# Optimization experiments

Hardware: AMD Instinct MI355X
Metric: run time of the kernel (lower is better)

## Reference

```python
import jax, jax.numpy as jnp
import numpy as np

G_GRID, K_SPLINE = 8, 3          # KAN grid size and spline order (k=3 in source)
N_GRAPHS = 512                    # graphs in the batched graph
NEG_SLOPE = 0.01                  # nn.LeakyReLU default

def _knots():
    # pykan-style grid on [-1,1] extended by k knots each side
    h = 2.0 / G_GRID
    base = jnp.linspace(-1.0, 1.0, G_GRID + 1)
    lo = -1.0 - h * jnp.arange(K_SPLINE, 0, -1, dtype=jnp.float32)
    hi = 1.0 + h * jnp.arange(1, K_SPLINE + 1, dtype=jnp.float32)
    return jnp.concatenate([lo, base, hi])  # [G + 2k + 1]

def _bspline(x, knots):
    # Cox-de Boor recursion. x: [N, D] -> basis [N, D, G + k]
    xx = x[..., None]
    b = ((xx >= knots[:-1]) & (xx < knots[1:])).astype(x.dtype)
    for d in range(1, K_SPLINE + 1):
        left = (xx - knots[:-(d + 1)]) / (knots[d:-1] - knots[:-(d + 1)]) * b[..., :-1]
        right = (knots[d + 1:] - xx) / (knots[d + 1:] - knots[1:-d]) * b[..., 1:]
        b = left + right
    return b

def _kan_layer(x, coef, sb, ss, knots):
    # phi(x)_o = sum_i sb[i,o]*silu(x_i) + ss[i,o]*sum_c coef[i,o,c]*B_c(x_i)
    B = _bspline(x, knots)                               # [N, in, C]
    return jnp.einsum('nic,ioc->no', B, coef * ss[:, :, None]) + jax.nn.silu(x) @ sb

def setup_inputs() -> dict:
    key = jax.random.key(0)
    ks = jax.random.split(key, 24)
    N, E, IN, HID, OUT, MID, C = 100000, 1600000, 64, 128, 1, 5, G_GRID + K_SPLINE
    def p(k, shape, s=0.1):
        return jax.random.normal(k, shape, jnp.float32) * s
    inp = {}
    inp['h'] = jax.random.normal(ks[0], (N, IN), jnp.float32) * 0.5
    inp['src'] = jax.random.randint(ks[1], (E,), 0, N)
    inp['dst'] = jax.random.randint(ks[2], (E,), 0, N)
    inp['gid'] = jnp.sort(jax.random.randint(ks[3], (N,), 0, N_GRAPHS))
    # KAN encoder: width=[IN, 5, HID]
    inp['coef1'] = p(ks[4], (IN, MID, C)); inp['sb1'] = p(ks[5], (IN, MID)); inp['ss1'] = p(ks[6], (IN, MID))
    inp['coef2'] = p(ks[7], (MID, HID, C)); inp['sb2'] = p(ks[8], (MID, HID)); inp['ss2'] = p(ks[9], (MID, HID))
    # two SAGEConv('mean') layers
    inp['Ws0'] = p(ks[10], (HID, HID)); inp['Wn0'] = p(ks[11], (HID, HID)); inp['b0'] = jnp.zeros((HID,), jnp.float32)
    inp['Ws1'] = p(ks[12], (HID, HID)); inp['Wn1'] = p(ks[13], (HID, HID)); inp['b1'] = jnp.zeros((HID,), jnp.float32)
    # KAN readout: width=[HID, 5, OUT]
    inp['coefr1'] = p(ks[14], (HID, MID, C)); inp['sbr1'] = p(ks[15], (HID, MID)); inp['ssr1'] = p(ks[16], (HID, MID))
    inp['coefr2'] = p(ks[17], (MID, OUT, C)); inp['sbr2'] = p(ks[18], (MID, OUT)); inp['ssr2'] = p(ks[19], (MID, OUT))
    return inp

def reference(h, src, dst, gid, coef1, sb1, ss1, coef2, sb2, ss2,
              Ws0, Wn0, b0, Ws1, Wn1, b1,
              coefr1, sbr1, ssr1, coefr2, sbr2, ssr2):
    knots = _knots()
    N = h.shape[0]
    # KAN spline encoder: [N, IN] -> [N, 5] -> [N, HID]
    h = _kan_layer(_kan_layer(h, coef1, sb1, ss1, knots), coef2, sb2, ss2, knots)
    # in-degree for mean aggregation (zero-degree nodes get 0 neighbor message)
    deg = jnp.maximum(jax.ops.segment_sum(jnp.ones(src.shape, h.dtype), dst, num_segments=N), 1.0)[:, None]
    for Ws, Wn, b in ((Ws0, Wn0, b0), (Ws1, Wn1, b1)):
        mean_n = jax.ops.segment_sum(h[src], dst, num_segments=N) / deg   # gather + mean-scatter
        z = h @ Ws + mean_n @ Wn + b + h                                   # SAGEConv + residual
        h = jnp.where(z > 0, z, NEG_SLOPE * z)                             # leaky_relu
    # average pooling per graph
    cnt = jnp.maximum(jax.ops.segment_sum(jnp.ones((N,), h.dtype), gid, num_segments=N_GRAPHS), 1.0)[:, None]
    y = jax.ops.segment_sum(h, gid, num_segments=N_GRAPHS) / cnt           # [G, HID]
    # KAN readout + sigmoid
    y = _kan_layer(_kan_layer(y, coefr1, sbr1, ssr1, knots), coefr2, sbr2, ssr2, knots)
    return jax.nn.sigmoid(y)
```

## Files before the change

### kernel.cpp

```cpp
#include <hip/hip_runtime.h>


#define IN_F   64
#define MID_F  5
#define HID_F  128
#define NG     512
#define NC     11
#define NJ     14
#define NXCD   8
#define PGRID  1024

typedef __attribute__((ext_vector_type(8))) __bf16 bf16x8;
typedef __attribute__((ext_vector_type(4))) float  f32x4;

__device__ __forceinline__ void bspline11(float x, float* __restrict__ B) {
    float b[14];
#pragma unroll
    for (int j = 0; j < 14; ++j) {
        float tj = -1.75f + 0.25f * j;
        b[j] = (x >= tj && x < tj + 0.25f) ? 1.0f : 0.0f;
    }
#pragma unroll
    for (int d = 1; d <= 3; ++d) {
        float inv = 1.0f / (0.25f * d);
#pragma unroll 14
        for (int j = 0; j < 14 - 3; ++j) {
            if (j < 14 - d) {
                float tj   = -1.75f + 0.25f * j;
                float tjd1 = tj + 0.25f * (d + 1);
                b[j] = ((x - tj) * b[j] + (tjd1 - x) * b[j + 1]) * inv;
            }
        }
        if (d < 3) {
#pragma unroll
            for (int j = 11; j < 14; ++j) {
                if (j < 14 - d) {
                    float tj   = -1.75f + 0.25f * j;
                    float tjd1 = tj + 0.25f * (d + 1);
                    b[j] = ((x - tj) * b[j] + (tjd1 - x) * b[j + 1]) * inv;
                }
            }
        }
    }
#pragma unroll
    for (int j = 0; j < NC; ++j) B[j] = b[j];
}

__device__ __forceinline__ float silu_f(float x) { return x / (1.0f + expf(-x)); }

__device__ __forceinline__ float4 poly_from_coefs(float c0, float c1, float c2, float c3) {
    const float s = 1.0f / 6.0f;
    float4 p;
    p.x = (-c0 + 3.f*c1 - 3.f*c2 + c3) * s;
    p.y = ( 3.f*c0 - 6.f*c1 + 3.f*c2) * s;
    p.z = (-3.f*c0 + 3.f*c2) * s;
    p.w = (      c0 + 4.f*c1 + c2) * s;
    return p;
}

__global__ __launch_bounds__(256) void build_poly1_kernel(
    const float* __restrict__ coef1, const float* __restrict__ ss1,
    float* __restrict__ poly1)
{
    int idx = blockIdx.x * 256 + threadIdx.x;
    if (idx >= IN_F * NJ * MID_F) return;
    int o = idx % MID_F;
    int t = idx / MID_F;
    int j = t % NJ;
    int i = t / NJ;
    float ss = ss1[i * MID_F + o];
    float c[4];
#pragma unroll
    for (int k = 0; k < 4; ++k) {
        int cc = j - 3 + k;
        c[k] = (cc >= 0 && cc <= 10) ? coef1[(i * MID_F + o) * NC + cc] * ss : 0.f;
    }
    *(float4*)(poly1 + (size_t)idx * 4) = poly_from_coefs(c[0], c[1], c[2], c[3]);
}

__global__ __launch_bounds__(256) void build_poly2_kernel(
    const float* __restrict__ coef2, const float* __restrict__ ss2,
    float* __restrict__ poly2)
{
    int idx = blockIdx.x * 256 + threadIdx.x;
    if (idx >= MID_F * NJ * HID_F) return;
    int o = idx & 127;
    int t = idx >> 7;
    int j = t % NJ;
    int i = t / NJ;
    float ss = ss2[i * HID_F + o];
    float c[4];
#pragma unroll
    for (int k = 0; k < 4; ++k) {
        int cc = j - 3 + k;
        c[k] = (cc >= 0 && cc <= 10) ? coef2[(i * HID_F + o) * NC + cc] * ss : 0.f;
    }
    *(float4*)(poly2 + (size_t)idx * 4) = poly_from_coefs(c[0], c[1], c[2], c[3]);
}

__global__ __launch_bounds__(256) void build_wfrag_kernel(
    const float* __restrict__ Ws0, const float* __restrict__ Wn0,
    const float* __restrict__ Ws1, const float* __restrict__ Wn1,
    unsigned short* __restrict__ wfrag0, unsigned short* __restrict__ wfrag1)
{
    int t = blockIdx.x * 256 + threadIdx.x;
    if (t >= 2 * 256 * HID_F) return;
    int layer = t >> 15;
    int e = t & 32767;
    int col = e & 127;
    int k   = e >> 7;
    int ks  = k >> 5;
    int kin = k & 31;
    int lg  = kin >> 3;
    int j   = kin & 7;
    int c   = col >> 4;
    int li  = col & 15;
    int l   = lg * 16 + li;
    const float* Ws = layer ? Ws1 : Ws0;
    const float* Wn = layer ? Wn1 : Wn0;
    float v = (k < HID_F) ? Ws[k * HID_F + col] : Wn[(k - HID_F) * HID_F + col];
    unsigned short us = __builtin_bit_cast(unsigned short, (__bf16)v);
    unsigned short* dst = layer ? wfrag1 : wfrag0;
    dst[((ks * 8 + c) * 64 + l) * 8 + j] = us;
}

__global__ __launch_bounds__(256) void enc1_kernel(
    const float* __restrict__ h, const float* __restrict__ poly1,
    const float* __restrict__ sb1, float* __restrict__ mid, int N)
{
    __shared__ float s_sb[IN_F * MID_F];
    for (int idx = threadIdx.x; idx < IN_F * MID_F; idx += 256)
        s_sb[idx] = sb1[idx];
    __syncthreads();

    int n = blockIdx.x * 256 + threadIdx.x;
    if (n >= N) return;
    const float* hr = h + (size_t)n * IN_F;
    float acc[MID_F] = {0, 0, 0, 0, 0};

#pragma unroll 4
    for (int i4 = 0; i4 < IN_F; i4 += 4) {
        float4 xv = *(const float4*)(hr + i4);
        float xs[4] = {xv.x, xv.y, xv.z, xv.w};
#pragma unroll
        for (int k = 0; k < 4; ++k) {
            int i = i4 + k;
            float x = xs[k];
            float xf = (x + 1.75f) * 4.0f;
            float fj = floorf(xf);
            int j0 = (int)fj;
            j0 = j0 < 0 ? 0 : (j0 > 13 ? 13 : j0);
            float u = xf - fj;
            float msk = (x >= -1.75f && x < 1.75f) ? 1.0f : 0.0f;
            float s = silu_f(x);
            const float* pp = poly1 + ((size_t)(i * NJ + j0) * MID_F) * 4;
#pragma unroll
            for (int o = 0; o < MID_F; ++o) {
                float4 p = *(const float4*)(pp + 4 * o);
                float t = fmaf(fmaf(fmaf(p.x, u, p.y), u, p.z), u, p.w);
                acc[o] = fmaf(s_sb[i * MID_F + o], s, acc[o]);
                acc[o] = fmaf(t, msk, acc[o]);
            }
        }
    }
#pragma unroll
    for (int o = 0; o < MID_F; ++o) mid[(size_t)n * MID_F + o] = acc[o];
}

__global__ __launch_bounds__(256) void enc2_kernel(
    const float* __restrict__ mid, const float* __restrict__ poly2,
    const float* __restrict__ sb2, float* __restrict__ h0,
    unsigned short* __restrict__ hb, int N)
{
    __shared__ float s_u[2][MID_F], s_sil[2][MID_F], s_msk[2][MID_F];
    __shared__ int   s_j0[2][MID_F];
    int o  = threadIdx.x & 127;
    int ln = threadIdx.x >> 7;

    float sbr[MID_F];
#pragma unroll
    for (int i = 0; i < MID_F; ++i) sbr[i] = sb2[i * HID_F + o];

    int nTiles = (N + 1) / 2;
    for (int tile = blockIdx.x; tile < nTiles; tile += gridDim.x) {
        __syncthreads();
        if (threadIdx.x < 2 * MID_F) {
            int l = threadIdx.x / MID_F, i = threadIdx.x % MID_F;
            int n = tile * 2 + l;
            float x = (n < N) ? mid[(size_t)n * MID_F + i] : 0.f;
            float xf = (x + 1.75f) * 4.0f;
            float fj = floorf(xf);
            int j0 = (int)fj;
            j0 = j0 < 0 ? 0 : (j0 > 13 ? 13 : j0);
            s_j0[l][i]  = j0;
            s_u[l][i]   = xf - fj;
            s_msk[l][i] = (x >= -1.75f && x < 1.75f) ? 1.0f : 0.0f;
            s_sil[l][i] = silu_f(x);
        }
        __syncthreads();
        int n = tile * 2 + ln;
        if (n < N) {
            float z = 0.f;
#pragma unroll
            for (int i = 0; i < MID_F; ++i) {
                float4 p = *(const float4*)(poly2 +
                            ((size_t)((i * NJ + s_j0[ln][i]) * HID_F + o)) * 4);
                float u = s_u[ln][i];
                float t = fmaf(fmaf(fmaf(p.x, u, p.y), u, p.z), u, p.w);
                z = fmaf(sbr[i], s_sil[ln][i], z);
                z = fmaf(t, s_msk[ln][i], z);
            }
            h0[(size_t)n * HID_F + o] = z;
            hb[(size_t)n * HID_F + o] =
                __builtin_bit_cast(unsigned short, (__bf16)z);
        }
    }
}

__global__ __launch_bounds__(256) void count8_kernel(
    const int* __restrict__ dst, int* __restrict__ cnt, int E, int psz)
{
    int part = blockIdx.x & (NXCD - 1);
    int q    = blockIdx.x >> 3;
    int plo = part * psz, phi = plo + psz;
    const int stride = (PGRID >> 3) * 256 * 4;
    for (int e0 = (q * 256 + threadIdx.x) * 4; e0 < E; e0 += stride) {
        if (e0 + 3 < E) {
            int4 d4 = *(const int4*)(dst + e0);
            if (d4.x >= plo && d4.x < phi) atomicAdd(&cnt[d4.x], 1);
            if (d4.y >= plo && d4.y < phi) atomicAdd(&cnt[d4.y], 1);
            if (d4.z >= plo && d4.z < phi) atomicAdd(&cnt[d4.z], 1);
            if (d4.w >= plo && d4.w < phi) atomicAdd(&cnt[d4.w], 1);
        } else {
            for (int k = 0; k < 4 && e0 + k < E; ++k) {
                int d = dst[e0 + k];
                if (d >= plo && d < phi) atomicAdd(&cnt[d], 1);
            }
        }
    }
}

__global__ __launch_bounds__(256) void scan1_kernel(
    const int* __restrict__ cnt, int* __restrict__ offs,
    int* __restrict__ bsum, int N)
{
    __shared__ int s[256];
    int base = blockIdx.x * 1024 + threadIdx.x * 4;
    int v0 = (base + 0 < N) ? cnt[base + 0] : 0;
    int v1 = (base + 1 < N) ? cnt[base + 1] : 0;
    int v2 = (base + 2 < N) ? cnt[base + 2] : 0;
    int v3 = (base + 3 < N) ? cnt[base + 3] : 0;
    int tsum = v0 + v1 + v2 + v3;
    s[threadIdx.x] = tsum;
    __syncthreads();
    for (int off = 1; off < 256; off <<= 1) {
        int t = 0;
        if (threadIdx.x >= off) t = s[threadIdx.x - off];
        __syncthreads();
        if (threadIdx.x >= off) s[threadIdx.x] += t;
        __syncthreads();
    }
    int p = s[threadIdx.x] - tsum;
    if (threadIdx.x == 255) bsum[blockIdx.x] = s[255];
    if (base + 0 < N) { offs[base + 0] = p; p += v0; }
    if (base + 1 < N) { offs[base + 1] = p; p += v1; }
    if (base + 2 < N) { offs[base + 2] = p; p += v2; }
    if (base + 3 < N) { offs[base + 3] = p; p += v3; }
}

__global__ __launch_bounds__(256) void scan2_kernel(int* __restrict__ bsum, int nblk)
{
    __shared__ int s[256];
    int v = (threadIdx.x < nblk) ? bsum[threadIdx.x] : 0;
    s[threadIdx.x] = v;
    __syncthreads();
    for (int off = 1; off < 256; off <<= 1) {
        int t = 0;
        if (threadIdx.x >= off) t = s[threadIdx.x - off];
        __syncthreads();
        if (threadIdx.x >= off) s[threadIdx.x] += t;
        __syncthreads();
    }
    if (threadIdx.x < nblk) bsum[threadIdx.x] = s[threadIdx.x] - v;
}

__global__ __launch_bounds__(256) void scan3_kernel(
    int* __restrict__ offs, const int* __restrict__ bsum, int N, int E)
{
    int i = blockIdx.x * 256 + threadIdx.x;
    if (i < N) offs[i] += bsum[i >> 10];
    if (i == 0) offs[N] = E;
}

__global__ __launch_bounds__(256) void fill8_kernel(
    const int* __restrict__ src, const int* __restrict__ dst,
    const int* __restrict__ offs, int* __restrict__ cursor,
    int* __restrict__ csr, int E, int psz)
{
    int part = blockIdx.x & (NXCD - 1);
    int q    = blockIdx.x >> 3;
    int plo = part * psz, phi = plo + psz;
    const int stride = (PGRID >> 3) * 256 * 4;
    for (int e0 = (q * 256 + threadIdx.x) * 4; e0 < E; e0 += stride) {
        if (e0 + 3 < E) {
            int4 d4 = *(const int4*)(dst + e0);
            int4 s4 = *(const int4*)(src + e0);
            if (d4.x >= plo && d4.x < phi) { int p = atomicAdd(&cursor[d4.x], 1); csr[offs[d4.x] + p] = s4.x; }
            if (d4.y >= plo && d4.y < phi) { int p = atomicAdd(&cursor[d4.y], 1); csr[offs[d4.y] + p] = s4.y; }
            if (d4.z >= plo && d4.z < phi) { int p = atomicAdd(&cursor[d4.z], 1); csr[offs[d4.z] + p] = s4.z; }
            if (d4.w >= plo && d4.w < phi) { int p = atomicAdd(&cursor[d4.w], 1); csr[offs[d4.w] + p] = s4.w; }
        } else {
            for (int k = 0; k < 4 && e0 + k < E; ++k) {
                int d = dst[e0 + k];
                if (d >= plo && d < phi) {
                    int p = atomicAdd(&cursor[d], 1);
                    csr[offs[d] + p] = src[e0 + k];
                }
            }
        }
    }
}

__global__ __launch_bounds__(256) void agg_kernel(
    const unsigned short* __restrict__ hb, const int* __restrict__ csr,
    const int* __restrict__ offs, unsigned short* __restrict__ meanb, int N)
{
    int wid  = (blockIdx.x * 256 + threadIdx.x) >> 6;
    int lane = threadIdx.x & 63;
    if (wid >= N) return;
    int lo = offs[wid], hi = offs[wid + 1];
    float ax = 0.f, ay = 0.f;
    for (int base = lo; base < hi; base += 64) {
        int m = hi - base;
        int idx = 0;
        if (lane < m) idx = csr[base + lane];
        int cnt = m < 64 ? m : 64;
        int j = 0;
        for (; j + 3 < cnt; j += 4) {
            int s0 = __shfl(idx, j + 0);
            int s1 = __shfl(idx, j + 1);
            int s2 = __shfl(idx, j + 2);
            int s3 = __shfl(idx, j + 3);
            unsigned int v0 = *(const unsigned int*)(hb + (size_t)s0 * HID_F + lane * 2);
            unsigned int v1 = *(const unsigned int*)(hb + (size_t)s1 * HID_F + lane * 2);
            unsigned int v2 = *(const unsigned int*)(hb + (size_t)s2 * HID_F + lane * 2);
            unsigned int v3 = *(const unsigned int*)(hb + (size_t)s3 * HID_F + lane * 2);
            ax += __builtin_bit_cast(float, v0 << 16) + __builtin_bit_cast(float, v1 << 16)
                + __builtin_bit_cast(float, v2 << 16) + __builtin_bit_cast(float, v3 << 16);
            ay += __builtin_bit_cast(float, v0 & 0xffff0000u) + __builtin_bit_cast(float, v1 & 0xffff0000u)
                + __builtin_bit_cast(float, v2 & 0xffff0000u) + __builtin_bit_cast(float, v3 & 0xffff0000u);
        }
        for (; j < cnt; ++j) {
            int s0 = __shfl(idx, j);
            unsigned int v0 = *(const unsigned int*)(hb + (size_t)s0 * HID_F + lane * 2);
            ax += __builtin_bit_cast(float, v0 << 16);
            ay += __builtin_bit_cast(float, v0 & 0xffff0000u);
        }
    }
    float inv = (hi > lo) ? 1.0f / (float)(hi - lo) : 0.0f;
    unsigned short ux = __builtin_bit_cast(unsigned short, (__bf16)(ax * inv));
    unsigned short uy = __builtin_bit_cast(unsigned short, (__bf16)(ay * inv));
    *(unsigned int*)(meanb + (size_t)wid * HID_F + lane * 2) =
        (unsigned int)ux | ((unsigned int)uy << 16);
}

__global__ __launch_bounds__(256) void sage_mfma_kernel(
    const unsigned short* __restrict__ hb, const unsigned short* __restrict__ meanb,
    const float* __restrict__ hres, const unsigned short* __restrict__ wfrag,
    const float* __restrict__ bias, float* __restrict__ hout,
    unsigned short* __restrict__ hbout, int N)
{
    int wv = threadIdx.x >> 6;
    int l  = threadIdx.x & 63;
    int n0 = blockIdx.x * 64 + wv * 16;
    int r  = l & 15;
    int kg = l >> 4;

    const uint4* rowh = (const uint4*)(hb    + (size_t)(n0 + r) * HID_F);
    const uint4* rowm = (const uint4*)(meanb + (size_t)(n0 + r) * HID_F);
    const uint4* wp   = (const uint4*)wfrag + l;

    f32x4 acc[8] = {};
#pragma unroll
    for (int ks = 0; ks < 8; ++ks) {
        uint4 av = (ks < 4) ? rowh[ks * 4 + kg] : rowm[(ks - 4) * 4 + kg];
        bf16x8 a = __builtin_bit_cast(bf16x8, av);
#pragma unroll
        for (int c = 0; c < 8; ++c) {
            uint4 w = wp[(ks * 8 + c) * 64];
            bf16x8 b = __builtin_bit_cast(bf16x8, w);
            acc[c] = __builtin_amdgcn_mfma_f32_16x16x32_bf16(a, b, acc[c], 0, 0, 0);
        }
    }

    int row0 = kg * 4;
#pragma unroll
    for (int c = 0; c < 8; ++c) {
        int col = c * 16 + r;
        float bv = bias[col];
#pragma unroll
        for (int rr = 0; rr < 4; ++rr) {
            int grow = n0 + row0 + rr;
            if (grow < N) {
                float z = acc[c][rr] + bv + hres[(size_t)grow * HID_F + col];
                z = z > 0.f ? z : 0.01f * z;
                hout[(size_t)grow * HID_F + col] = z;
                if (hbout)
                    hbout[(size_t)grow * HID_F + col] =
                        __builtin_bit_cast(unsigned short, (__bf16)z);
            }
        }
    }
}

__global__ __launch_bounds__(512) void pool_readout1_kernel(
    const float* __restrict__ h, const int* __restrict__ gid,
    const float* __restrict__ coefr1, const float* __restrict__ sbr1,
    const float* __restrict__ ssr1, float* __restrict__ ymid, int N)
{
    int g = blockIdx.x;
    int tid = threadIdx.x;
    __shared__ int s_lo, s_hi;
    if (tid == 0) {
        int lo = 0, hi = N;
        while (lo < hi) { int m = (lo + hi) >> 1; if (gid[m] < g) lo = m + 1; else hi = m; }
        s_lo = lo;
        int lo2 = lo, hi2 = N;
        while (lo2 < hi2) { int m = (lo2 + hi2) >> 1; if (gid[m] < g + 1) lo2 = m + 1; else hi2 = m; }
        s_hi = lo2;
    }
    __syncthreads();
    int lo = s_lo, hi = s_hi;

    int ro = tid >> 5;
    int c4 = (tid & 31) * 4;
    float4 a = {0.f, 0.f, 0.f, 0.f};
    for (int n = lo + ro; n < hi; n += 16) {
        float4 v = *(const float4*)(h + (size_t)n * HID_F + c4);
        a.x += v.x; a.y += v.y; a.z += v.z; a.w += v.w;
    }
    __shared__ float s_acc[16][HID_F];
    *(float4*)(&s_acc[ro][c4]) = a;
    __syncthreads();

    __shared__ float s_part[2][MID_F];
    float p[MID_F];
    int i = tid;
    if (tid < HID_F) {
        float acc = 0.f;
#pragma unroll
        for (int r = 0; r < 16; ++r) acc += s_acc[r][i];
        float x = acc * (1.0f / fmaxf((float)(hi - lo), 1.0f));

        float B[NC];
        bspline11(x, B);
        float s = silu_f(x);
        const float* cp  = coefr1 + (size_t)i * (MID_F * NC);
        const float* ssp = ssr1 + (size_t)i * MID_F;
        const float* sbp = sbr1 + (size_t)i * MID_F;
#pragma unroll
        for (int o = 0; o < MID_F; ++o) {
            float t = 0.f;
#pragma unroll
            for (int c = 0; c < NC; ++c) t = fmaf(cp[o * NC + c], B[c], t);
            p[o] = sbp[o] * s + ssp[o] * t;
        }
#pragma unroll
        for (int off = 32; off >= 1; off >>= 1) {
#pragma unroll
            for (int o = 0; o < MID_F; ++o) p[o] += __shfl_down(p[o], off);
        }
        int lane = tid & 63, w = tid >> 6;
        if (lane == 0) {
#pragma unroll
            for (int o = 0; o < MID_F; ++o) s_part[w][o] = p[o];
        }
    }
    __syncthreads();
    if (tid < MID_F)
        ymid[g * MID_F + tid] = s_part[0][tid] + s_part[1][tid];
}

__global__ __launch_bounds__(256) void readout2_kernel(
    const float* __restrict__ ymid, const float* __restrict__ coefr2,
    const float* __restrict__ sbr2, const float* __restrict__ ssr2,
    float* __restrict__ out)
{
    int g = blockIdx.x * 256 + threadIdx.x;
    if (g >= NG) return;
    float acc = 0.f;
#pragma unroll
    for (int i = 0; i < MID_F; ++i) {
        float x = ymid[g * MID_F + i];
        float B[NC];
        bspline11(x, B);
        float t = 0.f;
#pragma unroll
        for (int c = 0; c < NC; ++c) t = fmaf(coefr2[i * NC + c], B[c], t);
        acc += sbr2[i] * silu_f(x) + ssr2[i] * t;
    }
    out[g] = 1.0f / (1.0f + expf(-acc));
}

extern "C" void kernel_launch(void* const* d_in, const int* in_sizes, int n_in,
                              void* d_out, int out_size, void* d_ws, size_t ws_size,
                              hipStream_t stream)
{
    const float* h     = (const float*)d_in[0];
    const int*   src   = (const int*)d_in[1];
    const int*   dst   = (const int*)d_in[2];
    const int*   gid   = (const int*)d_in[3];
    const float* coef1 = (const float*)d_in[4];
    const float* sb1   = (const float*)d_in[5];
    const float* ss1   = (const float*)d_in[6];
    const float* coef2 = (const float*)d_in[7];
    const float* sb2   = (const float*)d_in[8];
    const float* ss2   = (const float*)d_in[9];
    const float* Ws0   = (const float*)d_in[10];
    const float* Wn0   = (const float*)d_in[11];
    const float* b0    = (const float*)d_in[12];
    const float* Ws1   = (const float*)d_in[13];
    const float* Wn1   = (const float*)d_in[14];
    const float* b1    = (const float*)d_in[15];
    const float* coefr1= (const float*)d_in[16];
    const float* sbr1  = (const float*)d_in[17];
    const float* ssr1  = (const float*)d_in[18];
    const float* coefr2= (const float*)d_in[19];
    const float* sbr2  = (const float*)d_in[20];
    const float* ssr2  = (const float*)d_in[21];

    const int N = in_sizes[0] / IN_F;
    const int E = in_sizes[1];

    float* ws   = (float*)d_ws;
    float* mid  = ws;
    float* h0   = mid + (size_t)N * MID_F;
    float* h1   = h0 + (size_t)N * HID_F;
    unsigned short* meanb = (unsigned short*)(h1 + (size_t)N * HID_F);
    unsigned short* hb    = meanb + (size_t)N * HID_F;
    float* ymid = (float*)(hb + (size_t)N * HID_F);
    unsigned short* wfrag0 = (unsigned short*)(ymid + NG * MID_F);
    unsigned short* wfrag1 = wfrag0 + 32768;
    int*   cnt  = (int*)(wfrag1 + 32768);
    int*   offs = cnt + N;
    int*   bsum = offs + N + 1;
    int*   csr  = bsum + 256;

    float* poly1 = (float*)meanb;
    float* poly2 = poly1 + IN_F * NJ * MID_F * 4;

    const int nblk = (N + 1023) / 1024;
    const int psz  = (N + NXCD - 1) / NXCD;

    build_poly1_kernel<<<(IN_F * NJ * MID_F + 255) / 256, 256, 0, stream>>>(coef1, ss1, poly1);
    build_poly2_kernel<<<(MID_F * NJ * HID_F + 255) / 256, 256, 0, stream>>>(coef2, ss2, poly2);
    build_wfrag_kernel<<<(2 * 256 * HID_F + 255) / 256, 256, 0, stream>>>(
        Ws0, Wn0, Ws1, Wn1, wfrag0, wfrag1);

    enc1_kernel<<<(N + 255) / 256, 256, 0, stream>>>(h, poly1, sb1, mid, N);
    enc2_kernel<<<2048, 256, 0, stream>>>(mid, poly2, sb2, h0, hb, N);

    hipMemsetAsync(cnt, 0, (size_t)N * sizeof(int), stream);
    count8_kernel<<<PGRID, 256, 0, stream>>>(dst, cnt, E, psz);
    scan1_kernel<<<nblk, 256, 0, stream>>>(cnt, offs, bsum, N);
    scan2_kernel<<<1, 256, 0, stream>>>(bsum, nblk);
    scan3_kernel<<<(N + 255) / 256, 256, 0, stream>>>(offs, bsum, N, E);
    hipMemsetAsync(cnt, 0, (size_t)N * sizeof(int), stream);
    fill8_kernel<<<PGRID, 256, 0, stream>>>(src, dst, offs, cnt, csr, E, psz);

    agg_kernel<<<(N * 64 + 255) / 256, 256, 0, stream>>>(hb, csr, offs, meanb, N);
    sage_mfma_kernel<<<(N + 63) / 64, 256, 0, stream>>>(
        hb, meanb, h0, wfrag0, b0, h1, hb, N);

    agg_kernel<<<(N * 64 + 255) / 256, 256, 0, stream>>>(hb, csr, offs, meanb, N);
    sage_mfma_kernel<<<(N + 63) / 64, 256, 0, stream>>>(
        hb, meanb, h1, wfrag1, b1, h0, (unsigned short*)nullptr, N);

    pool_readout1_kernel<<<NG, 512, 0, stream>>>(h0, gid, coefr1, sbr1, ssr1, ymid, N);
    readout2_kernel<<<2, 256, 0, stream>>>(ymid, coefr2, sbr2, ssr2, (float*)d_out);
}
```

Measured before the change: 589.9 us.

## Drop fp32 hidden-state copies, keep bf16 only; reuse counts as fill cursors

Removes the fp32 h0/h1 buffers. The encoder, SAGE layers and pooling now read and write only the bf16 hidden state, updated in place, with the residual taken from bf16. The fill kernel decrements the degree counts as cursors, which removes the second memset. The aggregation inner loop is also unrolled to 8 gathers. This cuts memory traffic on the fp32 residual reads and writes, but the residual and the pooling input lose precision because they now pass through bf16.

```diff
diff --git a/kernel.cpp b/kernel.cpp
--- a/kernel.cpp
+++ b/kernel.cpp
@@ -12,6 +12,10 @@
 
 typedef __attribute__((ext_vector_type(8))) __bf16 bf16x8;
 typedef __attribute__((ext_vector_type(4))) float  f32x4;
+
+__device__ __forceinline__ float bf2f(unsigned short u) {
+    return __builtin_bit_cast(float, ((unsigned int)u) << 16);
+}
 
 __device__ __forceinline__ void bspline11(float x, float* __restrict__ B) {
     float b[14];
@@ -169,8 +173,7 @@
 
 __global__ __launch_bounds__(256) void enc2_kernel(
     const float* __restrict__ mid, const float* __restrict__ poly2,
-    const float* __restrict__ sb2, float* __restrict__ h0,
-    unsigned short* __restrict__ hb, int N)
+    const float* __restrict__ sb2, unsigned short* __restrict__ hb, int N)
 {
     __shared__ float s_u[2][MID_F], s_sil[2][MID_F], s_msk[2][MID_F];
     __shared__ int   s_j0[2][MID_F];
@@ -210,7 +213,6 @@
                 z = fmaf(sbr[i], s_sil[ln][i], z);
                 z = fmaf(t, s_msk[ln][i], z);
             }
-            h0[(size_t)n * HID_F + o] = z;
             hb[(size_t)n * HID_F + o] =
                 __builtin_bit_cast(unsigned short, (__bf16)z);
         }
@@ -294,7 +296,7 @@
 
 __global__ __launch_bounds__(256) void fill8_kernel(
     const int* __restrict__ src, const int* __restrict__ dst,
-    const int* __restrict__ offs, int* __restrict__ cursor,
+    const int* __restrict__ offs, int* __restrict__ cnt,
     int* __restrict__ csr, int E, int psz)
 {
     int part = blockIdx.x & (NXCD - 1);
@@ -305,15 +307,15 @@
         if (e0 + 3 < E) {
             int4 d4 = *(const int4*)(dst + e0);
             int4 s4 = *(const int4*)(src + e0);
-            if (d4.x >= plo && d4.x < phi) { int p = atomicAdd(&cursor[d4.x], 1); csr[offs[d4.x] + p] = s4.x; }
-            if (d4.y >= plo && d4.y < phi) { int p = atomicAdd(&cursor[d4.y], 1); csr[offs[d4.y] + p] = s4.y; }
-            if (d4.z >= plo && d4.z < phi) { int p = atomicAdd(&cursor[d4.z], 1); csr[offs[d4.z] + p] = s4.z; }
-            if (d4.w >= plo && d4.w < phi) { int p = atomicAdd(&cursor[d4.w], 1); csr[offs[d4.w] + p] = s4.w; }
+            if (d4.x >= plo && d4.x < phi) { int p = atomicSub(&cnt[d4.x], 1) - 1; csr[offs[d4.x] + p] = s4.x; }
+            if (d4.y >= plo && d4.y < phi) { int p = atomicSub(&cnt[d4.y], 1) - 1; csr[offs[d4.y] + p] = s4.y; }
+            if (d4.z >= plo && d4.z < phi) { int p = atomicSub(&cnt[d4.z], 1) - 1; csr[offs[d4.z] + p] = s4.z; }
+            if (d4.w >= plo && d4.w < phi) { int p = atomicSub(&cnt[d4.w], 1) - 1; csr[offs[d4.w] + p] = s4.w; }
         } else {
             for (int k = 0; k < 4 && e0 + k < E; ++k) {
                 int d = dst[e0 + k];
                 if (d >= plo && d < phi) {
-                    int p = atomicAdd(&cursor[d], 1);
+                    int p = atomicSub(&cnt[d], 1) - 1;
                     csr[offs[d] + p] = src[e0 + k];
                 }
             }
@@ -336,19 +338,18 @@
         if (lane < m) idx = csr[base + lane];
         int cnt = m < 64 ? m : 64;
         int j = 0;
-        for (; j + 3 < cnt; j += 4) {
-            int s0 = __shfl(idx, j + 0);
-            int s1 = __shfl(idx, j + 1);
-            int s2 = __shfl(idx, j + 2);
-            int s3 = __shfl(idx, j + 3);
-            unsigned int v0 = *(const unsigned int*)(hb + (size_t)s0 * HID_F + lane * 2);
-            unsigned int v1 = *(const unsigned int*)(hb + (size_t)s1 * HID_F + lane * 2);
-            unsigned int v2 = *(const unsigned int*)(hb + (size_t)s2 * HID_F + lane * 2);
-            unsigned int v3 = *(const unsigned int*)(hb + (size_t)s3 * HID_F + lane * 2);
-            ax += __builtin_bit_cast(float, v0 << 16) + __builtin_bit_cast(float, v1 << 16)
-                + __builtin_bit_cast(float, v2 << 16) + __builtin_bit_cast(float, v3 << 16);
-            ay += __builtin_bit_cast(float, v0 & 0xffff0000u) + __builtin_bit_cast(float, v1 & 0xffff0000u)
-                + __builtin_bit_cast(float, v2 & 0xffff0000u) + __builtin_bit_cast(float, v3 & 0xffff0000u);
+        for (; j + 7 < cnt; j += 8) {
+            unsigned int v[8];
+#pragma unroll
+            for (int k = 0; k < 8; ++k) {
+                int s = __shfl(idx, j + k);
+                v[k] = *(const unsigned int*)(hb + (size_t)s * HID_F + lane * 2);
+            }
+#pragma unroll
+            for (int k = 0; k < 8; ++k) {
+                ax += __builtin_bit_cast(float, v[k] << 16);
+                ay += __builtin_bit_cast(float, v[k] & 0xffff0000u);
+            }
         }
         for (; j < cnt; ++j) {
             int s0 = __shfl(idx, j);
@@ -365,10 +366,9 @@
 }
 
 __global__ __launch_bounds__(256) void sage_mfma_kernel(
-    const unsigned short* __restrict__ hb, const unsigned short* __restrict__ meanb,
-    const float* __restrict__ hres, const unsigned short* __restrict__ wfrag,
-    const float* __restrict__ bias, float* __restrict__ hout,
-    unsigned short* __restrict__ hbout, int N)
+    unsigned short* __restrict__ hb, const unsigned short* __restrict__ meanb,
+    const unsigned short* __restrict__ wfrag, const float* __restrict__ bias,
+    int N)
 {
     int wv = threadIdx.x >> 6;
     int l  = threadIdx.x & 63;
@@ -402,19 +402,17 @@
         for (int rr = 0; rr < 4; ++rr) {
             int grow = n0 + row0 + rr;
             if (grow < N) {
-                float z = acc[c][rr] + bv + hres[(size_t)grow * HID_F + col];
+                size_t off = (size_t)grow * HID_F + col;
+                float z = acc[c][rr] + bv + bf2f(hb[off]);
                 z = z > 0.f ? z : 0.01f * z;
-                hout[(size_t)grow * HID_F + col] = z;
-                if (hbout)
-                    hbout[(size_t)grow * HID_F + col] =
-                        __builtin_bit_cast(unsigned short, (__bf16)z);
+                hb[off] = __builtin_bit_cast(unsigned short, (__bf16)z);
             }
         }
     }
 }
 
 __global__ __launch_bounds__(512) void pool_readout1_kernel(
-    const float* __restrict__ h, const int* __restrict__ gid,
+    const unsigned short* __restrict__ hb, const int* __restrict__ gid,
     const float* __restrict__ coefr1, const float* __restrict__ sbr1,
     const float* __restrict__ ssr1, float* __restrict__ ymid, int N)
 {
@@ -434,13 +432,19 @@
 
     int ro = tid >> 5;
     int c4 = (tid & 31) * 4;
-    float4 a = {0.f, 0.f, 0.f, 0.f};
+    float a0 = 0.f, a1 = 0.f, a2 = 0.f, a3 = 0.f;
     for (int n = lo + ro; n < hi; n += 16) {
-        float4 v = *(const float4*)(h + (size_t)n * HID_F + c4);
-        a.x += v.x; a.y += v.y; a.z += v.z; a.w += v.w;
+        uint2 v = *(const uint2*)(hb + (size_t)n * HID_F + c4);
+        a0 += __builtin_bit_cast(float, v.x << 16);
+        a1 += __builtin_bit_cast(float, v.x & 0xffff0000u);
+        a2 += __builtin_bit_cast(float, v.y << 16);
+        a3 += __builtin_bit_cast(float, v.y & 0xffff0000u);
     }
     __shared__ float s_acc[16][HID_F];
-    *(float4*)(&s_acc[ro][c4]) = a;
+    s_acc[ro][c4 + 0] = a0;
+    s_acc[ro][c4 + 1] = a1;
+    s_acc[ro][c4 + 2] = a2;
+    s_acc[ro][c4 + 3] = a3;
     __syncthreads();
 
     __shared__ float s_part[2][MID_F];
@@ -534,9 +538,7 @@
 
     float* ws   = (float*)d_ws;
     float* mid  = ws;
-    float* h0   = mid + (size_t)N * MID_F;
-    float* h1   = h0 + (size_t)N * HID_F;
-    unsigned short* meanb = (unsigned short*)(h1 + (size_t)N * HID_F);
+    unsigned short* meanb = (unsigned short*)(mid + (size_t)N * MID_F);
     unsigned short* hb    = meanb + (size_t)N * HID_F;
     float* ymid = (float*)(hb + (size_t)N * HID_F);
     unsigned short* wfrag0 = (unsigned short*)(ymid + NG * MID_F);
@@ -558,24 +560,21 @@
         Ws0, Wn0, Ws1, Wn1, wfrag0, wfrag1);
 
     enc1_kernel<<<(N + 255) / 256, 256, 0, stream>>>(h, poly1, sb1, mid, N);
-    enc2_kernel<<<2048, 256, 0, stream>>>(mid, poly2, sb2, h0, hb, N);
+    enc2_kernel<<<2048, 256, 0, stream>>>(mid, poly2, sb2, hb, N);
 
     hipMemsetAsync(cnt, 0, (size_t)N * sizeof(int), stream);
     count8_kernel<<<PGRID, 256, 0, stream>>>(dst, cnt, E, psz);
     scan1_kernel<<<nblk, 256, 0, stream>>>(cnt, offs, bsum, N);
     scan2_kernel<<<1, 256, 0, stream>>>(bsum, nblk);
     scan3_kernel<<<(N + 255) / 256, 256, 0, stream>>>(offs, bsum, N, E);
-    hipMemsetAsync(cnt, 0, (size_t)N * sizeof(int), stream);
     fill8_kernel<<<PGRID, 256, 0, stream>>>(src, dst, offs, cnt, csr, E, psz);
 
     agg_kernel<<<(N * 64 + 255) / 256, 256, 0, stream>>>(hb, csr, offs, meanb, N);
-    sage_mfma_kernel<<<(N + 63) / 64, 256, 0, stream>>>(
-        hb, meanb, h0, wfrag0, b0, h1, hb, N);
+    sage_mfma_kernel<<<(N + 63) / 64, 256, 0, stream>>>(hb, meanb, wfrag0, b0, N);
 
     agg_kernel<<<(N * 64 + 255) / 256, 256, 0, stream>>>(hb, csr, offs, meanb, N);
-    sage_mfma_kernel<<<(N + 63) / 64, 256, 0, stream>>>(
-        hb, meanb, h1, wfrag1, b1, h0, (unsigned short*)nullptr, N);
-
-    pool_readout1_kernel<<<NG, 512, 0, stream>>>(h0, gid, coefr1, sbr1, ssr1, ymid, N);
+    sage_mfma_kernel<<<(N + 63) / 64, 256, 0, stream>>>(hb, meanb, wfrag1, b1, N);
+
+    pool_readout1_kernel<<<NG, 512, 0, stream>>>(hb, gid, coefr1, sbr1, ssr1, ymid, N);
     readout2_kernel<<<2, 256, 0, stream>>>(ymid, coefr2, sbr2, ssr2, (float*)d_out);
 }
```

Result: faster. 556.5 us (-5.7%).
